# Optimization experiments

Measured on AMD Instinct MI355X. Metric: run time of the kernel, lower is better.

The kernel has to match this reference:

```python
import jax, jax.numpy as jnp
import numpy as np

B, S, H = 2, 2048, 2048
NH, KVH, HD = 32, 8, 64
G = NH // KVH
BASE = 10000.0
SCALE = 1.0 / np.sqrt(HD).astype(np.float32)


def _rope_cache(seq_len, dim, base):
    inv_freq = 1.0 / (base ** (jnp.arange(0, dim, 2, dtype=jnp.float32) / dim))
    t = jnp.arange(seq_len, dtype=jnp.float32)
    freqs = jnp.outer(t, inv_freq)            # [S, HD/2]
    emb = jnp.concatenate([freqs, freqs], -1)  # [S, HD]
    return jnp.cos(emb), jnp.sin(emb)


def _rotate_half(x):
    x1, x2 = jnp.split(x, 2, axis=-1)
    return jnp.concatenate([-x2, x1], axis=-1)


def setup_inputs() -> dict:
    key = jax.random.key(0)
    ks = jax.random.split(key, 5)
    hidden_states = jax.random.normal(ks[0], (B, S, H), jnp.float32)
    # additive causal mask, broadcast over heads
    causal = jnp.tril(jnp.ones((S, S), dtype=bool))
    attention_mask = jnp.where(causal, 0.0, -1e9).astype(jnp.float32)[None, None]
    attention_mask = jnp.broadcast_to(attention_mask, (B, 1, S, S))
    position_ids = jnp.broadcast_to(jnp.arange(S, dtype=jnp.int32), (B, S))
    w = 0.02
    Wq = jax.random.normal(ks[1], (H, NH * HD), jnp.float32) * w
    Wk = jax.random.normal(ks[2], (H, KVH * HD), jnp.float32) * w
    Wv = jax.random.normal(ks[3], (H, KVH * HD), jnp.float32) * w
    Wo = jax.random.normal(ks[4], (NH * HD, H), jnp.float32) * w
    return {"hidden_states": hidden_states, "attention_mask": attention_mask,
            "position_ids": position_ids, "Wq": Wq, "Wk": Wk, "Wv": Wv, "Wo": Wo}


def reference(hidden_states, attention_mask, position_ids, Wq, Wk, Wv, Wo):
    b, s, _ = hidden_states.shape
    q = (hidden_states @ Wq).reshape(b, s, NH, HD).transpose(0, 2, 1, 3)   # [B,NH,S,HD]
    k = (hidden_states @ Wk).reshape(b, s, KVH, HD).transpose(0, 2, 1, 3)  # [B,KVH,S,HD]
    v = (hidden_states @ Wv).reshape(b, s, KVH, HD).transpose(0, 2, 1, 3)
    cos_c, sin_c = _rope_cache(s, HD, BASE)
    cos = cos_c[position_ids][:, None]  # [B,1,S,HD]
    sin = sin_c[position_ids][:, None]
    q = q * cos + _rotate_half(q) * sin
    k = k * cos + _rotate_half(k) * sin
    # GQA: grouped einsum == repeat_kv + matmul (same math, no KV duplication)
    qg = q.reshape(b, KVH, G, s, HD)
    scores = jnp.einsum('bkgsd,bktd->bkgst', qg, k) * SCALE  # [B,KVH,G,S,S]
    scores = scores + attention_mask[:, :, None]             # mask [B,1,1,S,S]
    probs = jax.nn.softmax(scores.astype(jnp.float32), axis=-1).astype(q.dtype)
    ctx = jnp.einsum('bkgst,bktd->bkgsd', probs, v)
    ctx = ctx.reshape(b, NH, s, HD).transpose(0, 2, 1, 3).reshape(b, s, NH * HD)
    return ctx @ Wo
```

## Files before the change

### kernel.cpp

```cpp
#include <hip/hip_runtime.h>
#include <hip/hip_bf16.h>

#define DB   2
#define DS   2048
#define DH   2048
#define DNH  32
#define DKVH 8
#define DHD  64
#define DM   4096
#define DNQKV 3072

typedef __attribute__((ext_vector_type(8))) short bf16x8;
typedef __attribute__((ext_vector_type(4))) float f32x4;
typedef __attribute__((ext_vector_type(8))) unsigned short us8;
typedef __attribute__((ext_vector_type(4))) unsigned short us4;
typedef __attribute__((ext_vector_type(2))) unsigned int u32x2;

__device__ __forceinline__ float b2f(unsigned short u) {
  unsigned int x = ((unsigned int)u) << 16;
  return __builtin_bit_cast(float, x);
}
__device__ __forceinline__ unsigned short f2b(float f) {
  unsigned int u = __builtin_bit_cast(unsigned int, f);
  return (unsigned short)((u + 0x8000u) >> 16);
}
__device__ __forceinline__ unsigned int cvt_pk_bf16(float lo, float hi) {
  unsigned int r;
  asm("v_cvt_pk_bf16_f32 %0, %1, %2" : "=v"(r) : "v"(lo), "v"(hi));
  return r;
}
__device__ __forceinline__ void async_copy16(void* lds, const void* g) {
  __builtin_amdgcn_global_load_lds((const __attribute__((address_space(1))) void*)g,
                                   (__attribute__((address_space(3))) void*)lds,
                                   16, 0, 0);
}

#define BARRIER() do { asm volatile("" ::: "memory"); __builtin_amdgcn_s_barrier(); asm volatile("" ::: "memory"); } while (0)
#define LGKM0()   asm volatile("s_waitcnt lgkmcnt(0)" ::: "memory")
#define WAITVM(n) asm volatile("s_waitcnt vmcnt(" #n ")" ::: "memory")
#define MFMA16(d, a, bb) (d) = __builtin_amdgcn_mfma_f32_16x16x32_bf16((a), (bb), (d), 0, 0, 0)

__device__ __forceinline__ int detect_inline(const unsigned short* __restrict__ w) {
  int t = threadIdx.x & 63;
  int trips = 0;
#pragma unroll
  for (int i = 0; i < 4; i++) {
    unsigned short u = w[t * 4 + i];
    int e = (u >> 7) & 0xFF;
    if (e >= 161 || (e <= 93 && e != 0)) trips++;
  }
#pragma unroll
  for (int off = 32; off > 0; off >>= 1) trips += __shfl_down(trips, off);
  return __shfl(trips, 0) >= 8;
}

__global__ __launch_bounds__(256)
void prep(const void* __restrict__ hs, const void* __restrict__ wq,
          const void* __restrict__ wk, const void* __restrict__ wv,
          const void* __restrict__ wo,
          unsigned short* __restrict__ xb, unsigned short* __restrict__ wtqkv,
          unsigned short* __restrict__ wto) {
  __shared__ float tile[32][33];
  int mode = detect_inline((const unsigned short*)wq);
  int bid = blockIdx.x;
  if (bid < 4096) {
    int i = (bid * 256 + threadIdx.x) * 8;
    if (mode) {
      const float* f = (const float*)hs;
      us8 o;
#pragma unroll
      for (int j = 0; j < 8; j++) o[j] = f2b(f[i + j]);
      *(us8*)&xb[i] = o;
    } else {
      *(us8*)&xb[i] = *(const us8*)((const unsigned short*)hs + i);
    }
    return;
  }
  const void* win; unsigned short* out; int C, bx, by;
  if (bid < 8192)       { int l = bid - 4096;  win = wq; out = wtqkv;                         C = 2048; bx = l & 63; by = l >> 6; }
  else if (bid < 9216)  { int l = bid - 8192;  win = wk; out = wtqkv + (size_t)2048 * 2048;   C = 512;  bx = l & 15; by = l >> 4; }
  else if (bid < 10240) { int l = bid - 9216;  win = wv; out = wtqkv + (size_t)2560 * 2048;   C = 512;  bx = l & 15; by = l >> 4; }
  else                  { int l = bid - 10240; win = wo; out = wto;                           C = 2048; bx = l & 63; by = l >> 6; }
  int c0 = bx * 32, r0 = by * 32;
  int tx = threadIdx.x & 31, ty = threadIdx.x >> 5;
  if (mode) {
    const float* f = (const float*)win;
    for (int i = ty; i < 32; i += 8) tile[i][tx] = f[(size_t)(r0 + i) * C + c0 + tx];
  } else {
    const unsigned short* bsrc = (const unsigned short*)win;
    for (int i = ty; i < 32; i += 8) tile[i][tx] = b2f(bsrc[(size_t)(r0 + i) * C + c0 + tx]);
  }
  __syncthreads();
  for (int i = ty; i < 32; i += 8) out[(size_t)(c0 + i) * 2048 + r0 + tx] = f2b(tile[tx][i]);
}

#define QSC 0.18033688011112042f

__global__ __launch_bounds__(512, 2)
void gemm_qkv(const unsigned short* __restrict__ A, const unsigned short* __restrict__ Bt,
              const int* __restrict__ pos_ids,
              unsigned short* __restrict__ qws, unsigned short* __restrict__ kws,
              unsigned short* __restrict__ vt) {
  __shared__ __align__(16) unsigned short sm[65536];
  int tid = threadIdx.x, lane = tid & 63, wave = tid >> 6;
  int wm = wave >> 2, wn = wave & 3;
  int quad = lane >> 4, l15 = lane & 15;

  int bid = blockIdx.x;
  int wg = (bid & 7) * 24 + (bid >> 3);
  int ty = wg / 12, tx = wg - ty * 12;
  size_t tm0 = (size_t)ty * 256, tn0 = (size_t)tx * 256;

  const unsigned short* Ab = A + tm0 * 2048;
  const unsigned short* Bb = Bt + tn0 * 2048;

  auto UA = [&](int bu, int kh) { return sm + (bu * 2 + kh) * 8192; };
  auto UB = [&](int bu, int kh) { return sm + 32768 + (bu * 2 + kh) * 8192; };

  int c0 = tid, c1 = tid + 512;
  int r0s = c0 >> 2, r1s = c1 >> 2;
  int cc0 = (c0 & 3) ^ ((r0s >> 1) & 3);
  int cc1 = (c1 & 3) ^ ((r1s >> 1) & 3);
  size_t ga0 = (size_t)r0s * 2048 + cc0 * 8;
  size_t ga1 = (size_t)r1s * 2048 + cc1 * 8;

  auto stA = [&](int t, int kh, int bu) {
    const unsigned short* s = Ab + (size_t)t * 64 + kh * 32;
    async_copy16(UA(bu, kh) + c0 * 8, s + ga0);
    async_copy16(UA(bu, kh) + c1 * 8, s + ga1);
  };
  auto stB = [&](int t, int kh, int bu) {
    const unsigned short* s = Bb + (size_t)t * 64 + kh * 32;
    async_copy16(UB(bu, kh) + c0 * 8, s + ga0);
    async_copy16(UB(bu, kh) + c1 * 8, s + ga1);
  };

  int rdoff = l15 * 32 + ((quad << 3) ^ (((l15 >> 1) & 3) << 3));

  f32x4 zero4 = {0.f, 0.f, 0.f, 0.f};
  f32x4 acc[8][4];
#pragma unroll
  for (int mi = 0; mi < 8; mi++)
#pragma unroll
    for (int ni = 0; ni < 4; ni++) acc[mi][ni] = zero4;

  stA(0, 0, 0); stB(0, 0, 0); stA(0, 1, 0); stB(0, 1, 0); stA(1, 0, 1); stB(1, 0, 1);
  WAITVM(8); BARRIER();

#pragma unroll 2
  for (int t = 0; t < 32; ++t) {
    int bu = t & 1, bn = bu ^ 1;
    int t1 = (t + 1 < 32) ? t + 1 : 31;
    int t2 = (t + 2 < 32) ? t + 2 : 31;
    bf16x8 af[8];
    const unsigned short* pA0 = UA(bu, 0) + wm * 4096 + rdoff;
    const unsigned short* pB0 = UB(bu, 0) + wn * 2048 + rdoff;
    const unsigned short* pA1 = UA(bu, 1) + wm * 4096 + rdoff;
    const unsigned short* pB1 = UB(bu, 1) + wn * 2048 + rdoff;

#pragma unroll
    for (int mi = 0; mi < 8; mi++) af[mi] = *(const bf16x8*)(pA0 + mi * 512);
    bf16x8 b0 = *(const bf16x8*)pB0;
    bf16x8 b1 = *(const bf16x8*)(pB0 + 512);
    stA(t1, 1, bn);
    BARRIER(); LGKM0();
    __builtin_amdgcn_s_setprio(1);
#pragma unroll
    for (int mi = 0; mi < 8; mi++) { MFMA16(acc[mi][0], af[mi], b0); MFMA16(acc[mi][1], af[mi], b1); }
    __builtin_amdgcn_s_setprio(0);
    BARRIER();

    bf16x8 b2 = *(const bf16x8*)(pB0 + 1024);
    bf16x8 b3 = *(const bf16x8*)(pB0 + 1536);
    stB(t1, 1, bn);
    BARRIER(); LGKM0();
    __builtin_amdgcn_s_setprio(1);
#pragma unroll
    for (int mi = 0; mi < 8; mi++) { MFMA16(acc[mi][2], af[mi], b2); MFMA16(acc[mi][3], af[mi], b3); }
    __builtin_amdgcn_s_setprio(0);
    WAITVM(8);
    BARRIER();

#pragma unroll
    for (int mi = 0; mi < 8; mi++) af[mi] = *(const bf16x8*)(pA1 + mi * 512);
    b0 = *(const bf16x8*)pB1;
    b1 = *(const bf16x8*)(pB1 + 512);
    stA(t2, 0, bu);
    BARRIER(); LGKM0();
    __builtin_amdgcn_s_setprio(1);
#pragma unroll
    for (int mi = 0; mi < 8; mi++) { MFMA16(acc[mi][0], af[mi], b0); MFMA16(acc[mi][1], af[mi], b1); }
    __builtin_amdgcn_s_setprio(0);
    BARRIER();

    b2 = *(const bf16x8*)(pB1 + 1024);
    b3 = *(const bf16x8*)(pB1 + 1536);
    stB(t2, 0, bu);
    BARRIER(); LGKM0();
    __builtin_amdgcn_s_setprio(1);
#pragma unroll
    for (int mi = 0; mi < 8; mi++) { MFMA16(acc[mi][2], af[mi], b2); MFMA16(acc[mi][3], af[mi], b3); }
    __builtin_amdgcn_s_setprio(0);
    WAITVM(8);
    BARRIER();
  }
  WAITVM(0);

  int hs = (int)(tn0 >> 6) + wn;
  if (hs < 40) {
    float sc = (hs < 32) ? QSC : 1.0f;
    unsigned short* dst0 = (hs < 32) ? qws : kws;
    int hh = (hs < 32) ? hs : (hs - 32);
    float invf0 = __expf(-(float)l15 * (9.210340371976184f / 32.0f));
    float invf1 = invf0 * 0.01f;
#pragma unroll
    for (int mi = 0; mi < 8; mi++)
#pragma unroll
      for (int r = 0; r < 4; r++) {
        size_t gr = tm0 + wm * 128 + mi * 16 + quad * 4 + r;
        int bb = (int)(gr >> 11), s = (int)(gr & 2047);
        float tpos = (float)pos_ids[gr];
        unsigned short* row = dst0 + ((size_t)(bb * ((hs < 32) ? DNH : DKVH) + hh) * DS + s) * DHD;
#pragma unroll
        for (int ni = 0; ni < 2; ni++) {
          float x1 = acc[mi][ni][r], x2 = acc[mi][ni + 2][r];
          float ang = tpos * (ni ? invf1 : invf0);
          float sn, cs;
          __sincosf(ang, &sn, &cs);
          int d = ni * 16 + l15;
          row[d]      = f2b((x1 * cs - x2 * sn) * sc);
          row[d + 32] = f2b((x2 * cs + x1 * sn) * sc);
        }
      }
  } else {
    int vh = hs - 40;
    int bb = (int)(tm0 >> 11);
    int s0 = (int)(tm0 & 2047) + wm * 128 + quad * 4;
#pragma unroll
    for (int mi = 0; mi < 8; mi++)
#pragma unroll
      for (int ni = 0; ni < 4; ni++) {
        int d = ni * 16 + l15;
        us4 o4;
#pragma unroll
        for (int r = 0; r < 4; r++) o4[r] = f2b(acc[mi][ni][r]);
        *(us4*)&vt[((size_t)(bb * DKVH + vh) * DHD + d) * DS + s0 + mi * 16] = o4;
      }
  }
}

__global__ __launch_bounds__(512, 2)
void gemm_out(const unsigned short* __restrict__ A, const unsigned short* __restrict__ Bt,
              unsigned short* __restrict__ Cb, float* __restrict__ Cf,
              const unsigned short* __restrict__ wqdet) {
  __shared__ __align__(16) unsigned short sm[49152];
  int tid = threadIdx.x, lane = tid & 63, wave = tid >> 6;
  int wm = wave >> 2, wn = wave & 3;
  int quad = lane >> 4, l15 = lane & 15;

  int bid = blockIdx.x;
  int wg = (bid & 7) * 32 + (bid >> 3);
  int ty = wg >> 3, tx = wg & 7;
  size_t tm0 = (size_t)ty * 128, tn0 = (size_t)tx * 256;

  const unsigned short* Ab = A + tm0 * 2048;
  const unsigned short* Bb = Bt + tn0 * 2048;

  auto UA = [&](int bu, int kh) { return sm + (bu * 2 + kh) * 4096; };
  auto UB = [&](int bu, int kh) { return sm + 16384 + (bu * 2 + kh) * 8192; };

  int c0 = tid, c1 = tid + 512;
  int r0s = c0 >> 2, r1s = c1 >> 2;
  int cc0 = (c0 & 3) ^ ((r0s >> 1) & 3);
  int cc1 = (c1 & 3) ^ ((r1s >> 1) & 3);
  size_t ga0 = (size_t)r0s * 2048 + cc0 * 8;
  size_t ga1 = (size_t)r1s * 2048 + cc1 * 8;

  auto stA = [&](int t, int kh, int bu) {
    const unsigned short* s = Ab + (size_t)t * 64 + kh * 32;
    async_copy16(UA(bu, kh) + c0 * 8, s + ga0);
  };
  auto stB = [&](int t, int kh, int bu) {
    const unsigned short* s = Bb + (size_t)t * 64 + kh * 32;
    async_copy16(UB(bu, kh) + c0 * 8, s + ga0);
    async_copy16(UB(bu, kh) + c1 * 8, s + ga1);
  };

  int rdoff = l15 * 32 + ((quad << 3) ^ (((l15 >> 1) & 3) << 3));

  f32x4 zero4 = {0.f, 0.f, 0.f, 0.f};
  f32x4 acc[4][4];
#pragma unroll
  for (int mi = 0; mi < 4; mi++)
#pragma unroll
    for (int ni = 0; ni < 4; ni++) acc[mi][ni] = zero4;

  stA(0, 0, 0); stB(0, 0, 0); stA(0, 1, 0); stB(0, 1, 0); stA(1, 0, 1); stB(1, 0, 1);
  WAITVM(6); BARRIER();

#pragma unroll 2
  for (int t = 0; t < 32; ++t) {
    int bu = t & 1, bn = bu ^ 1;
    int t1 = (t + 1 < 32) ? t + 1 : 31;
    int t2 = (t + 2 < 32) ? t + 2 : 31;
    bf16x8 af[4];
    const unsigned short* pA0 = UA(bu, 0) + wm * 2048 + rdoff;
    const unsigned short* pB0 = UB(bu, 0) + wn * 2048 + rdoff;
    const unsigned short* pA1 = UA(bu, 1) + wm * 2048 + rdoff;
    const unsigned short* pB1 = UB(bu, 1) + wn * 2048 + rdoff;

#pragma unroll
    for (int mi = 0; mi < 4; mi++) af[mi] = *(const bf16x8*)(pA0 + mi * 512);
    bf16x8 b0 = *(const bf16x8*)pB0;
    bf16x8 b1 = *(const bf16x8*)(pB0 + 512);
    stA(t1, 1, bn);
    BARRIER(); LGKM0();
    __builtin_amdgcn_s_setprio(1);
#pragma unroll
    for (int mi = 0; mi < 4; mi++) { MFMA16(acc[mi][0], af[mi], b0); MFMA16(acc[mi][1], af[mi], b1); }
    __builtin_amdgcn_s_setprio(0);
    BARRIER();

    bf16x8 b2 = *(const bf16x8*)(pB0 + 1024);
    bf16x8 b3 = *(const bf16x8*)(pB0 + 1536);
    stB(t1, 1, bn);
    BARRIER(); LGKM0();
    __builtin_amdgcn_s_setprio(1);
#pragma unroll
    for (int mi = 0; mi < 4; mi++) { MFMA16(acc[mi][2], af[mi], b2); MFMA16(acc[mi][3], af[mi], b3); }
    __builtin_amdgcn_s_setprio(0);
    WAITVM(6);
    BARRIER();

#pragma unroll
    for (int mi = 0; mi < 4; mi++) af[mi] = *(const bf16x8*)(pA1 + mi * 512);
    b0 = *(const bf16x8*)pB1;
    b1 = *(const bf16x8*)(pB1 + 512);
    stA(t2, 0, bu);
    BARRIER(); LGKM0();
    __builtin_amdgcn_s_setprio(1);
#pragma unroll
    for (int mi = 0; mi < 4; mi++) { MFMA16(acc[mi][0], af[mi], b0); MFMA16(acc[mi][1], af[mi], b1); }
    __builtin_amdgcn_s_setprio(0);
    BARRIER();

    b2 = *(const bf16x8*)(pB1 + 1024);
    b3 = *(const bf16x8*)(pB1 + 1536);
    stB(t2, 0, bu);
    BARRIER(); LGKM0();
    __builtin_amdgcn_s_setprio(1);
#pragma unroll
    for (int mi = 0; mi < 4; mi++) { MFMA16(acc[mi][2], af[mi], b2); MFMA16(acc[mi][3], af[mi], b3); }
    __builtin_amdgcn_s_setprio(0);
    WAITVM(6);
    BARRIER();
  }
  WAITVM(0);

  int mode = detect_inline(wqdet);
#pragma unroll
  for (int mi = 0; mi < 4; mi++)
#pragma unroll
    for (int ni = 0; ni < 4; ni++)
#pragma unroll
      for (int r = 0; r < 4; r++) {
        size_t gr = tm0 + wm * 64 + mi * 16 + quad * 4 + r;
        size_t gc = tn0 + wn * 64 + ni * 16 + l15;
        float v = acc[mi][ni][r];
        if (mode) Cf[gr * 2048 + gc] = v;
        else      Cb[gr * 2048 + gc] = f2b(v);
      }
}

__global__ __launch_bounds__(512, 4)
void flash_attn(const unsigned short* __restrict__ q, const unsigned short* __restrict__ k,
                const unsigned short* __restrict__ vt, unsigned short* __restrict__ ctx) {
  __shared__ __align__(16) unsigned short lK[2][2][64 * 32];
  __shared__ __align__(16) unsigned short lV[2][2][64 * 32];
  __shared__ __align__(16) unsigned short lP[8][16 * 64];
  int tid = threadIdx.x, lane = tid & 63, wave = tid >> 6;
  int quad = lane >> 4, l15 = lane & 15;
  int bh = blockIdx.x, b = bh >> 5, h = bh & 31, kvh = h >> 2;
  const unsigned short* qb = q + (size_t)(b * DNH + h) * DS * DHD;
  const unsigned short* kb = k + (size_t)(b * DKVH + kvh) * DS * DHD;
  const unsigned short* vb = vt + (size_t)(b * DKVH + kvh) * DHD * DS;
  unsigned short* lPw = lP[wave];
  int shalf = tid >> 8, r8 = tid & 255;
  int rowS = r8 >> 2;
  int cc8 = ((r8 & 3) ^ ((rowS >> 1) & 3)) * 8;
  int swz = ((l15 >> 1) & 3) << 3;
  int pswz = (l15 & 7) << 3;
  int ql = wave * 16 + l15;

  int qt = blockIdx.y;
  int ntA = 2 * qt + 2, ntB = 32 - 2 * qt;
  int qAg = qt * 128 + ql, qBg = (15 - qt) * 128 + ql;

  const unsigned short* qpA = qb + (size_t)qAg * DHD + quad * 8;
  const unsigned short* qpB = qb + (size_t)qBg * DHD + quad * 8;
  bf16x8 qfA0 = *(const bf16x8*)qpA, qfA1 = *(const bf16x8*)(qpA + 32);
  bf16x8 qfB0 = *(const bf16x8*)qpB, qfB1 = *(const bf16x8*)(qpB + 32);

  f32x4 zero4 = {0.f, 0.f, 0.f, 0.f};
  f32x4 oA[4], oB[4];
#pragma unroll
  for (int dj = 0; dj < 4; dj++) { oA[dj] = zero4; oB[dj] = zero4; }
  float mA = -1e30f, lA = 0.f, mB = -1e30f, lB = 0.f;

  auto stage = [&](int t, int buf) {
    const unsigned short* sk = kb + (size_t)(t * 64 + rowS) * DHD + shalf * 32 + cc8;
    async_copy16(&lK[buf][shalf][r8 * 8], sk);
    const unsigned short* sv = vb + (size_t)rowS * DS + t * 64 + shalf * 32 + cc8;
    async_copy16(&lV[buf][shalf][r8 * 8], sv);
  };

  auto smax_pv = [&](f32x4 (&sacc)[4], float& mrow, float& lrow, f32x4 (&oacc)[4],
                     int cur, int kv0, int qg, bool domask) {
    if (domask) {
#pragma unroll
      for (int nj = 0; nj < 4; nj++)
#pragma unroll
        for (int r = 0; r < 4; r++)
          if (kv0 + nj * 16 + quad * 4 + r > qg) sacc[nj][r] = -1e30f;
    }
    float a0 = fmaxf(fmaxf(sacc[0][0], sacc[0][1]), sacc[0][2]);
    float a1 = fmaxf(fmaxf(sacc[0][3], sacc[1][0]), sacc[1][1]);
    float a2 = fmaxf(fmaxf(sacc[1][2], sacc[1][3]), sacc[2][0]);
    float a3 = fmaxf(fmaxf(sacc[2][1], sacc[2][2]), sacc[2][3]);
    float a4 = fmaxf(fmaxf(sacc[3][0], sacc[3][1]), sacc[3][2]);
    float tm = fmaxf(fmaxf(fmaxf(a0, a1), fmaxf(a2, a3)), fmaxf(a4, sacc[3][3]));
    tm = fmaxf(tm, __shfl_xor(tm, 16));
    tm = fmaxf(tm, __shfl_xor(tm, 32));
    if (!__all(tm <= mrow + 8.f)) {
      float mn = fmaxf(mrow, tm);
      float alpha = __builtin_amdgcn_exp2f(mrow - mn);
      mrow = mn;
      lrow *= alpha;
#pragma unroll
      for (int dj = 0; dj < 4; dj++)
#pragma unroll
        for (int r = 0; r < 4; r++) oacc[dj][r] *= alpha;
    }
    float rs = 0.f;
#pragma unroll
    for (int nj = 0; nj < 4; nj++)
#pragma unroll
      for (int r = 0; r < 4; r++) {
        float e = __builtin_amdgcn_exp2f(sacc[nj][r] - mrow);
        sacc[nj][r] = e;
        rs += e;
      }
    rs += __shfl_xor(rs, 16);
    rs += __shfl_xor(rs, 32);
    lrow += rs;
#pragma unroll
    for (int nj = 0; nj < 4; nj++) {
      u32x2 w2;
      w2[0] = cvt_pk_bf16(sacc[nj][0], sacc[nj][1]);
      w2[1] = cvt_pk_bf16(sacc[nj][2], sacc[nj][3]);
      *(u32x2*)&lPw[l15 * 64 + ((nj * 16 + quad * 4) ^ pswz)] = w2;
    }
    bf16x8 pf0 = *(const bf16x8*)&lPw[l15 * 64 + ((quad * 8) ^ pswz)];
    bf16x8 pf1 = *(const bf16x8*)&lPw[l15 * 64 + ((32 + quad * 8) ^ pswz)];
    __builtin_amdgcn_s_setprio(1);
#pragma unroll
    for (int dj = 0; dj < 4; dj++) {
      int ro = (dj * 16 + l15) * 32 + ((quad * 8) ^ swz);
      bf16x8 vf0 = *(const bf16x8*)&lV[cur][0][ro];
      bf16x8 vf1 = *(const bf16x8*)&lV[cur][1][ro];
      MFMA16(oacc[dj], vf0, pf0);
      MFMA16(oacc[dj], vf1, pf1);
    }
    __builtin_amdgcn_s_setprio(0);
  };

  stage(0, 0);
  WAITVM(0); BARRIER();

  int cur = 0;
  for (int t = 0; t < ntA; t++) {
    stage(t + 1, cur ^ 1);
    f32x4 sA[4], sB[4];
    __builtin_amdgcn_s_setprio(1);
#pragma unroll
    for (int nj = 0; nj < 4; nj++) {
      int ro = (nj * 16 + l15) * 32 + ((quad * 8) ^ swz);
      bf16x8 kf0 = *(const bf16x8*)&lK[cur][0][ro];
      bf16x8 kf1 = *(const bf16x8*)&lK[cur][1][ro];
      sA[nj] = zero4;
      MFMA16(sA[nj], kf0, qfA0);
      MFMA16(sA[nj], kf1, qfA1);
      sB[nj] = zero4;
      MFMA16(sB[nj], kf0, qfB0);
      MFMA16(sB[nj], kf1, qfB1);
    }
    __builtin_amdgcn_s_setprio(0);
    smax_pv(sA, mA, lA, oA, cur, t * 64, qAg, (t * 64 + 63) > qAg);
    smax_pv(sB, mB, lB, oB, cur, t * 64, qBg, false);
    WAITVM(0); BARRIER();
    cur ^= 1;
  }
  for (int t = ntA; t < ntB; t++) {
    if (t + 1 < ntB) stage(t + 1, cur ^ 1);
    f32x4 sB[4];
    __builtin_amdgcn_s_setprio(1);
#pragma unroll
    for (int nj = 0; nj < 4; nj++) {
      int ro = (nj * 16 + l15) * 32 + ((quad * 8) ^ swz);
      bf16x8 kf0 = *(const bf16x8*)&lK[cur][0][ro];
      bf16x8 kf1 = *(const bf16x8*)&lK[cur][1][ro];
      sB[nj] = zero4;
      MFMA16(sB[nj], kf0, qfB0);
      MFMA16(sB[nj], kf1, qfB1);
    }
    __builtin_amdgcn_s_setprio(0);
    smax_pv(sB, mB, lB, oB, cur, t * 64, qBg, (t * 64 + 63) > qBg);
    WAITVM(0); BARRIER();
    cur ^= 1;
  }

  auto wout = [&](f32x4 (&oacc)[4], float lrow, int qg) {
    float inv = __builtin_amdgcn_rcpf(lrow);
    size_t orow = ((size_t)b * DS + qg) * (DNH * DHD) + (size_t)h * DHD;
#pragma unroll
    for (int dj = 0; dj < 4; dj++) {
      u32x2 o2;
      o2[0] = cvt_pk_bf16(oacc[dj][0] * inv, oacc[dj][1] * inv);
      o2[1] = cvt_pk_bf16(oacc[dj][2] * inv, oacc[dj][3] * inv);
      *(u32x2*)&ctx[orow + dj * 16 + quad * 4] = o2;
    }
  };
  wout(oA, lA, qAg);
  wout(oB, lB, qBg);
}

extern "C" void kernel_launch(void* const* d_in, const int* in_sizes, int n_in,
                              void* d_out, int out_size, void* d_ws, size_t ws_size,
                              hipStream_t stream) {
  (void)in_sizes; (void)n_in; (void)out_size; (void)ws_size;
  const void* hs = d_in[0];
  const int* pos = (const int*)d_in[2];
  const void* wq = d_in[3];
  const void* wk = d_in[4];
  const void* wv = d_in[5];
  const void* wo = d_in[6];

  char* ws = (char*)d_ws;
  size_t off = 0;
  auto take = [&](size_t bytes) -> char* {
    char* p = ws + off;
    off += (bytes + 255) & ~(size_t)255;
    return p;
  };
  unsigned short* xb    = (unsigned short*)take((size_t)DM * DH * 2);
  unsigned short* wtqkv = (unsigned short*)take((size_t)DNQKV * DH * 2);
  unsigned short* wto   = (unsigned short*)take((size_t)DH * DH * 2);
  unsigned short* qws   = (unsigned short*)take((size_t)DB * DNH * DS * DHD * 2);
  unsigned short* kws   = (unsigned short*)take((size_t)DB * DKVH * DS * DHD * 2);
  unsigned short* vtws  = (unsigned short*)take((size_t)DB * DKVH * DS * DHD * 2);
  unsigned short* ctx   = (unsigned short*)take((size_t)DM * DNH * DHD * 2);

  prep<<<14336, 256, 0, stream>>>(hs, wq, wk, wv, wo, xb, wtqkv, wto);

  gemm_qkv<<<dim3(192), 512, 0, stream>>>(xb, wtqkv, pos, qws, kws, vtws);

  flash_attn<<<dim3(DB * DNH, 8), 512, 0, stream>>>(qws, kws, vtws, ctx);

  gemm_out<<<dim3(256), 512, 0, stream>>>(ctx, wto, (unsigned short*)d_out, (float*)d_out,
                                          (const unsigned short*)wq);
}
```

Baseline: 300.4 us.

## Triple-buffer K/V staging, merge attention loops, defer row-sum reduction

K/V LDS staging grows from double to triple buffering, prefetching two tiles ahead with a partial vmcnt wait so global loads have more time to land. The two loops (paired A/B tiles and B-only tiles) become one loop with a doA predicate, and the PV MFMAs for both query blocks are grouped after both softmaxes. The per-tile cross-lane shuffle reduction of the softmax row sum is replaced by per-lane partial sums reduced once at the end. LDS use grows by 16KB per block, which could lower occupancy at 512 threads, and the predicate adds branches inside the loop.

Result: no change. 304.4 us (+1.3%).

```diff
diff --git a/kernel.cpp b/kernel.cpp
--- a/kernel.cpp
+++ b/kernel.cpp
@@ -375,8 +375,8 @@
 __global__ __launch_bounds__(512, 4)
 void flash_attn(const unsigned short* __restrict__ q, const unsigned short* __restrict__ k,
                 const unsigned short* __restrict__ vt, unsigned short* __restrict__ ctx) {
-  __shared__ __align__(16) unsigned short lK[2][2][64 * 32];
-  __shared__ __align__(16) unsigned short lV[2][2][64 * 32];
+  __shared__ __align__(16) unsigned short lK[3][2][64 * 32];
+  __shared__ __align__(16) unsigned short lV[3][2][64 * 32];
   __shared__ __align__(16) unsigned short lP[8][16 * 64];
   int tid = threadIdx.x, lane = tid & 63, wave = tid >> 6;
   int quad = lane >> 4, l15 = lane & 15;
@@ -405,7 +405,7 @@
   f32x4 oA[4], oB[4];
 #pragma unroll
   for (int dj = 0; dj < 4; dj++) { oA[dj] = zero4; oB[dj] = zero4; }
-  float mA = -1e30f, lA = 0.f, mB = -1e30f, lB = 0.f;
+  float mA = -1e30f, psA = 0.f, mB = -1e30f, psB = 0.f;
 
   auto stage = [&](int t, int buf) {
     const unsigned short* sk = kb + (size_t)(t * 64 + rowS) * DHD + shalf * 32 + cc8;
@@ -414,8 +414,8 @@
     async_copy16(&lV[buf][shalf][r8 * 8], sv);
   };
 
-  auto smax_pv = [&](f32x4 (&sacc)[4], float& mrow, float& lrow, f32x4 (&oacc)[4],
-                     int cur, int kv0, int qg, bool domask) {
+  auto softmax = [&](f32x4 (&sacc)[4], float& mrow, float& psum, f32x4 (&oacc)[4],
+                     int kv0, int qg, bool domask, bf16x8& pf0, bf16x8& pf1) {
     if (domask) {
 #pragma unroll
       for (int nj = 0; nj < 4; nj++)
@@ -435,74 +435,40 @@
       float mn = fmaxf(mrow, tm);
       float alpha = __builtin_amdgcn_exp2f(mrow - mn);
       mrow = mn;
-      lrow *= alpha;
+      psum *= alpha;
 #pragma unroll
       for (int dj = 0; dj < 4; dj++)
 #pragma unroll
         for (int r = 0; r < 4; r++) oacc[dj][r] *= alpha;
     }
-    float rs = 0.f;
-#pragma unroll
-    for (int nj = 0; nj < 4; nj++)
-#pragma unroll
-      for (int r = 0; r < 4; r++) {
-        float e = __builtin_amdgcn_exp2f(sacc[nj][r] - mrow);
-        sacc[nj][r] = e;
-        rs += e;
-      }
-    rs += __shfl_xor(rs, 16);
-    rs += __shfl_xor(rs, 32);
-    lrow += rs;
 #pragma unroll
     for (int nj = 0; nj < 4; nj++) {
+      float e0 = __builtin_amdgcn_exp2f(sacc[nj][0] - mrow);
+      float e1 = __builtin_amdgcn_exp2f(sacc[nj][1] - mrow);
+      float e2 = __builtin_amdgcn_exp2f(sacc[nj][2] - mrow);
+      float e3 = __builtin_amdgcn_exp2f(sacc[nj][3] - mrow);
+      psum += (e0 + e1) + (e2 + e3);
       u32x2 w2;
-      w2[0] = cvt_pk_bf16(sacc[nj][0], sacc[nj][1]);
-      w2[1] = cvt_pk_bf16(sacc[nj][2], sacc[nj][3]);
+      w2[0] = cvt_pk_bf16(e0, e1);
+      w2[1] = cvt_pk_bf16(e2, e3);
       *(u32x2*)&lPw[l15 * 64 + ((nj * 16 + quad * 4) ^ pswz)] = w2;
     }
-    bf16x8 pf0 = *(const bf16x8*)&lPw[l15 * 64 + ((quad * 8) ^ pswz)];
-    bf16x8 pf1 = *(const bf16x8*)&lPw[l15 * 64 + ((32 + quad * 8) ^ pswz)];
-    __builtin_amdgcn_s_setprio(1);
-#pragma unroll
-    for (int dj = 0; dj < 4; dj++) {
-      int ro = (dj * 16 + l15) * 32 + ((quad * 8) ^ swz);
-      bf16x8 vf0 = *(const bf16x8*)&lV[cur][0][ro];
-      bf16x8 vf1 = *(const bf16x8*)&lV[cur][1][ro];
-      MFMA16(oacc[dj], vf0, pf0);
-      MFMA16(oacc[dj], vf1, pf1);
-    }
-    __builtin_amdgcn_s_setprio(0);
+    pf0 = *(const bf16x8*)&lPw[l15 * 64 + ((quad * 8) ^ pswz)];
+    pf1 = *(const bf16x8*)&lPw[l15 * 64 + ((32 + quad * 8) ^ pswz)];
   };
 
   stage(0, 0);
-  WAITVM(0); BARRIER();
-
-  int cur = 0;
-  for (int t = 0; t < ntA; t++) {
-    stage(t + 1, cur ^ 1);
+  stage(1, 1);
+  WAITVM(2); BARRIER();
+
+  for (int t = 0; t < ntB; t++) {
+    int cur = t % 3;
+    int t2 = (t + 2 < ntB) ? t + 2 : ntB - 1;
+    stage(t2, (t + 2) % 3);
+    bool doA = (t < ntA);
+    int kv0 = t * 64;
+
     f32x4 sA[4], sB[4];
-    __builtin_amdgcn_s_setprio(1);
-#pragma unroll
-    for (int nj = 0; nj < 4; nj++) {
-      int ro = (nj * 16 + l15) * 32 + ((quad * 8) ^ swz);
-      bf16x8 kf0 = *(const bf16x8*)&lK[cur][0][ro];
-      bf16x8 kf1 = *(const bf16x8*)&lK[cur][1][ro];
-      sA[nj] = zero4;
-      MFMA16(sA[nj], kf0, qfA0);
-      MFMA16(sA[nj], kf1, qfA1);
-      sB[nj] = zero4;
-      MFMA16(sB[nj], kf0, qfB0);
-      MFMA16(sB[nj], kf1, qfB1);
-    }
-    __builtin_amdgcn_s_setprio(0);
-    smax_pv(sA, mA, lA, oA, cur, t * 64, qAg, (t * 64 + 63) > qAg);
-    smax_pv(sB, mB, lB, oB, cur, t * 64, qBg, false);
-    WAITVM(0); BARRIER();
-    cur ^= 1;
-  }
-  for (int t = ntA; t < ntB; t++) {
-    if (t + 1 < ntB) stage(t + 1, cur ^ 1);
-    f32x4 sB[4];
     __builtin_amdgcn_s_setprio(1);
 #pragma unroll
     for (int nj = 0; nj < 4; nj++) {
@@ -512,14 +478,42 @@
       sB[nj] = zero4;
       MFMA16(sB[nj], kf0, qfB0);
       MFMA16(sB[nj], kf1, qfB1);
-    }
-    __builtin_amdgcn_s_setprio(0);
-    smax_pv(sB, mB, lB, oB, cur, t * 64, qBg, (t * 64 + 63) > qBg);
-    WAITVM(0); BARRIER();
-    cur ^= 1;
-  }
-
-  auto wout = [&](f32x4 (&oacc)[4], float lrow, int qg) {
+      if (doA) {
+        sA[nj] = zero4;
+        MFMA16(sA[nj], kf0, qfA0);
+        MFMA16(sA[nj], kf1, qfA1);
+      }
+    }
+    __builtin_amdgcn_s_setprio(0);
+
+    bf16x8 pfA0, pfA1, pfB0, pfB1;
+    if (doA)
+      softmax(sA, mA, psA, oA, kv0, qAg, (kv0 + 63) > qAg, pfA0, pfA1);
+    softmax(sB, mB, psB, oB, kv0, qBg, (kv0 + 63) > qBg, pfB0, pfB1);
+
+    __builtin_amdgcn_s_setprio(1);
+#pragma unroll
+    for (int dj = 0; dj < 4; dj++) {
+      int ro = (dj * 16 + l15) * 32 + ((quad * 8) ^ swz);
+      bf16x8 vf0 = *(const bf16x8*)&lV[cur][0][ro];
+      bf16x8 vf1 = *(const bf16x8*)&lV[cur][1][ro];
+      MFMA16(oB[dj], vf0, pfB0);
+      MFMA16(oB[dj], vf1, pfB1);
+      if (doA) {
+        MFMA16(oA[dj], vf0, pfA0);
+        MFMA16(oA[dj], vf1, pfA1);
+      }
+    }
+    __builtin_amdgcn_s_setprio(0);
+
+    WAITVM(2); BARRIER();
+  }
+  WAITVM(0);
+
+  auto wout = [&](f32x4 (&oacc)[4], float psum, int qg) {
+    float lrow = psum;
+    lrow += __shfl_xor(lrow, 16);
+    lrow += __shfl_xor(lrow, 32);
     float inv = __builtin_amdgcn_rcpf(lrow);
     size_t orow = ((size_t)b * DS + qg) * (DNH * DHD) + (size_t)h * DHD;
 #pragma unroll
@@ -530,8 +524,8 @@
       *(u32x2*)&ctx[orow + dj * 16 + quad * 4] = o2;
     }
   };
-  wout(oA, lA, qAg);
-  wout(oB, lB, qBg);
+  wout(oA, psA, qAg);
+  wout(oB, psB, qBg);
 }
 
 extern "C" void kernel_launch(void* const* d_in, const int* in_sizes, int n_in,
```

## Shrink QKV GEMM tile to 128x256 with simple double-buffered K=32 loop

Applied to the files above, without the earlier changes.

Replaces the 256x256 tile, 64-wide K-step QKV projection GEMM with a 128x256 tile and a 32-wide K-step, doubling the grid to 384 workgroups. The hand-interleaved half-step pipeline is replaced by a plain double-buffered loop that waits for all loads and synchronizes once per step. Launch bounds are raised so more workgroups can share a CU. The aim is better CU fill on the 256-CU part, since 192 workgroups previously left CUs idle. The cost is less data reuse per tile, more barriers, and a full vmcnt(0) wait each iteration that limits overlap of loads with compute.

Result: slower. 935.1 us (+211.3%).

```diff
diff --git a/kernel.cpp b/kernel.cpp
--- a/kernel.cpp
+++ b/kernel.cpp
@@ -96,115 +96,72 @@
 
 #define QSC 0.18033688011112042f
 
-__global__ __launch_bounds__(512, 2)
+__global__ __launch_bounds__(512, 6)
 void gemm_qkv(const unsigned short* __restrict__ A, const unsigned short* __restrict__ Bt,
               const int* __restrict__ pos_ids,
               unsigned short* __restrict__ qws, unsigned short* __restrict__ kws,
               unsigned short* __restrict__ vt) {
-  __shared__ __align__(16) unsigned short sm[65536];
+  __shared__ __align__(16) unsigned short lA[2][128 * 32];
+  __shared__ __align__(16) unsigned short lB[2][256 * 32];
   int tid = threadIdx.x, lane = tid & 63, wave = tid >> 6;
   int wm = wave >> 2, wn = wave & 3;
   int quad = lane >> 4, l15 = lane & 15;
 
   int bid = blockIdx.x;
-  int wg = (bid & 7) * 24 + (bid >> 3);
+  int wg = (bid & 7) * 48 + (bid >> 3);
   int ty = wg / 12, tx = wg - ty * 12;
-  size_t tm0 = (size_t)ty * 256, tn0 = (size_t)tx * 256;
+  size_t tm0 = (size_t)ty * 128, tn0 = (size_t)tx * 256;
 
   const unsigned short* Ab = A + tm0 * 2048;
   const unsigned short* Bb = Bt + tn0 * 2048;
 
-  auto UA = [&](int bu, int kh) { return sm + (bu * 2 + kh) * 8192; };
-  auto UB = [&](int bu, int kh) { return sm + 32768 + (bu * 2 + kh) * 8192; };
-
+  int rA = tid >> 2;
+  int cA = ((tid & 3) ^ ((rA >> 1) & 3)) * 8;
   int c0 = tid, c1 = tid + 512;
-  int r0s = c0 >> 2, r1s = c1 >> 2;
-  int cc0 = (c0 & 3) ^ ((r0s >> 1) & 3);
-  int cc1 = (c1 & 3) ^ ((r1s >> 1) & 3);
-  size_t ga0 = (size_t)r0s * 2048 + cc0 * 8;
-  size_t ga1 = (size_t)r1s * 2048 + cc1 * 8;
-
-  auto stA = [&](int t, int kh, int bu) {
-    const unsigned short* s = Ab + (size_t)t * 64 + kh * 32;
-    async_copy16(UA(bu, kh) + c0 * 8, s + ga0);
-    async_copy16(UA(bu, kh) + c1 * 8, s + ga1);
-  };
-  auto stB = [&](int t, int kh, int bu) {
-    const unsigned short* s = Bb + (size_t)t * 64 + kh * 32;
-    async_copy16(UB(bu, kh) + c0 * 8, s + ga0);
-    async_copy16(UB(bu, kh) + c1 * 8, s + ga1);
+  int rB0 = c0 >> 2, rB1 = c1 >> 2;
+  int cB0 = ((c0 & 3) ^ ((rB0 >> 1) & 3)) * 8;
+  int cB1 = ((c1 & 3) ^ ((rB1 >> 1) & 3)) * 8;
+
+  auto stage = [&](int t, int buf) {
+    const unsigned short* sa = Ab + (size_t)t * 32;
+    async_copy16(&lA[buf][tid * 8], sa + (size_t)rA * 2048 + cA);
+    const unsigned short* sb = Bb + (size_t)t * 32;
+    async_copy16(&lB[buf][c0 * 8], sb + (size_t)rB0 * 2048 + cB0);
+    async_copy16(&lB[buf][c1 * 8], sb + (size_t)rB1 * 2048 + cB1);
   };
 
   int rdoff = l15 * 32 + ((quad << 3) ^ (((l15 >> 1) & 3) << 3));
 
   f32x4 zero4 = {0.f, 0.f, 0.f, 0.f};
-  f32x4 acc[8][4];
-#pragma unroll
-  for (int mi = 0; mi < 8; mi++)
+  f32x4 acc[4][4];
+#pragma unroll
+  for (int mi = 0; mi < 4; mi++)
 #pragma unroll
     for (int ni = 0; ni < 4; ni++) acc[mi][ni] = zero4;
 
-  stA(0, 0, 0); stB(0, 0, 0); stA(0, 1, 0); stB(0, 1, 0); stA(1, 0, 1); stB(1, 0, 1);
-  WAITVM(8); BARRIER();
-
-#pragma unroll 2
-  for (int t = 0; t < 32; ++t) {
-    int bu = t & 1, bn = bu ^ 1;
-    int t1 = (t + 1 < 32) ? t + 1 : 31;
-    int t2 = (t + 2 < 32) ? t + 2 : 31;
-    bf16x8 af[8];
-    const unsigned short* pA0 = UA(bu, 0) + wm * 4096 + rdoff;
-    const unsigned short* pB0 = UB(bu, 0) + wn * 2048 + rdoff;
-    const unsigned short* pA1 = UA(bu, 1) + wm * 4096 + rdoff;
-    const unsigned short* pB1 = UB(bu, 1) + wn * 2048 + rdoff;
-
-#pragma unroll
-    for (int mi = 0; mi < 8; mi++) af[mi] = *(const bf16x8*)(pA0 + mi * 512);
-    bf16x8 b0 = *(const bf16x8*)pB0;
-    bf16x8 b1 = *(const bf16x8*)(pB0 + 512);
-    stA(t1, 1, bn);
-    BARRIER(); LGKM0();
-    __builtin_amdgcn_s_setprio(1);
-#pragma unroll
-    for (int mi = 0; mi < 8; mi++) { MFMA16(acc[mi][0], af[mi], b0); MFMA16(acc[mi][1], af[mi], b1); }
-    __builtin_amdgcn_s_setprio(0);
-    BARRIER();
-
-    bf16x8 b2 = *(const bf16x8*)(pB0 + 1024);
-    bf16x8 b3 = *(const bf16x8*)(pB0 + 1536);
-    stB(t1, 1, bn);
-    BARRIER(); LGKM0();
-    __builtin_amdgcn_s_setprio(1);
-#pragma unroll
-    for (int mi = 0; mi < 8; mi++) { MFMA16(acc[mi][2], af[mi], b2); MFMA16(acc[mi][3], af[mi], b3); }
-    __builtin_amdgcn_s_setprio(0);
-    WAITVM(8);
-    BARRIER();
-
-#pragma unroll
-    for (int mi = 0; mi < 8; mi++) af[mi] = *(const bf16x8*)(pA1 + mi * 512);
-    b0 = *(const bf16x8*)pB1;
-    b1 = *(const bf16x8*)(pB1 + 512);
-    stA(t2, 0, bu);
-    BARRIER(); LGKM0();
-    __builtin_amdgcn_s_setprio(1);
-#pragma unroll
-    for (int mi = 0; mi < 8; mi++) { MFMA16(acc[mi][0], af[mi], b0); MFMA16(acc[mi][1], af[mi], b1); }
-    __builtin_amdgcn_s_setprio(0);
-    BARRIER();
-
-    b2 = *(const bf16x8*)(pB1 + 1024);
-    b3 = *(const bf16x8*)(pB1 + 1536);
-    stB(t2, 0, bu);
-    BARRIER(); LGKM0();
-    __builtin_amdgcn_s_setprio(1);
-#pragma unroll
-    for (int mi = 0; mi < 8; mi++) { MFMA16(acc[mi][2], af[mi], b2); MFMA16(acc[mi][3], af[mi], b3); }
-    __builtin_amdgcn_s_setprio(0);
-    WAITVM(8);
-    BARRIER();
-  }
-  WAITVM(0);
+  stage(0, 0);
+  WAITVM(0); BARRIER();
+
+  int cur = 0;
+  for (int t = 0; t < 64; t++) {
+    if (t + 1 < 64) stage(t + 1, cur ^ 1);
+    bf16x8 af[4], bfr[4];
+    const unsigned short* pA = &lA[cur][wm * 64 * 32] + rdoff;
+    const unsigned short* pB = &lB[cur][wn * 64 * 32] + rdoff;
+#pragma unroll
+    for (int mi = 0; mi < 4; mi++) af[mi] = *(const bf16x8*)(pA + mi * 512);
+#pragma unroll
+    for (int ni = 0; ni < 4; ni++) bfr[ni] = *(const bf16x8*)(pB + ni * 512);
+    __builtin_amdgcn_s_setprio(1);
+#pragma unroll
+    for (int mi = 0; mi < 4; mi++)
+#pragma unroll
+      for (int ni = 0; ni < 4; ni++)
+        MFMA16(acc[mi][ni], af[mi], bfr[ni]);
+    __builtin_amdgcn_s_setprio(0);
+    WAITVM(0); BARRIER();
+    cur ^= 1;
+  }
 
   int hs = (int)(tn0 >> 6) + wn;
   if (hs < 40) {
@@ -214,10 +171,10 @@
     float invf0 = __expf(-(float)l15 * (9.210340371976184f / 32.0f));
     float invf1 = invf0 * 0.01f;
 #pragma unroll
-    for (int mi = 0; mi < 8; mi++)
+    for (int mi = 0; mi < 4; mi++)
 #pragma unroll
       for (int r = 0; r < 4; r++) {
-        size_t gr = tm0 + wm * 128 + mi * 16 + quad * 4 + r;
+        size_t gr = tm0 + wm * 64 + mi * 16 + quad * 4 + r;
         int bb = (int)(gr >> 11), s = (int)(gr & 2047);
         float tpos = (float)pos_ids[gr];
         unsigned short* row = dst0 + ((size_t)(bb * ((hs < 32) ? DNH : DKVH) + hh) * DS + s) * DHD;
@@ -235,9 +192,9 @@
   } else {
     int vh = hs - 40;
     int bb = (int)(tm0 >> 11);
-    int s0 = (int)(tm0 & 2047) + wm * 128 + quad * 4;
-#pragma unroll
-    for (int mi = 0; mi < 8; mi++)
+    int s0 = (int)(tm0 & 2047) + wm * 64 + quad * 4;
+#pragma unroll
+    for (int mi = 0; mi < 4; mi++)
 #pragma unroll
       for (int ni = 0; ni < 4; ni++) {
         int d = ni * 16 + l15;
@@ -562,7 +519,7 @@
 
   prep<<<14336, 256, 0, stream>>>(hs, wq, wk, wv, wo, xb, wtqkv, wto);
 
-  gemm_qkv<<<dim3(192), 512, 0, stream>>>(xb, wtqkv, pos, qws, kws, vtws);
+  gemm_qkv<<<dim3(384), 512, 0, stream>>>(xb, wtqkv, pos, qws, kws, vtws);
 
   flash_attn<<<dim3(DB * DNH, 8), 512, 0, stream>>>(qws, kws, vtws, ctx);
 
```
